# Kernel tuning notes

Hardware: AMD Instinct MI355X
Metric: run time of the kernel (lower is better)

The kernel has to match this reference:

```python
import jax, jax.numpy as jnp
import numpy as np

N = 50000      # nodes
F_IN = 2048    # raw node feature dim (pooled to 1024)
POOL = 1024
E = 1600000    # directed edges
E_SEL = 200000 # labeled edges for link prediction


def setup_inputs() -> dict:
    key = jax.random.key(0)
    ks = jax.random.split(key, 24)
    def lin(k, fin, fout):
        return jax.random.normal(k, (fin, fout), dtype=jnp.float32) / np.float32(np.sqrt(fin))
    inp = {
        "x": jax.random.normal(ks[0], (N, F_IN), dtype=jnp.float32),
        "edge_index": jax.random.randint(ks[1], (2, E), 0, N, dtype=jnp.int32),
        "mask": jax.random.randint(ks[2], (E_SEL,), 0, E, dtype=jnp.int32),
        "ln_g": jnp.ones((POOL,), jnp.float32),
        "ln_b": jnp.zeros((POOL,), jnp.float32),
        "w0": lin(ks[3], 1024, 512), "b0": jnp.zeros((512,), jnp.float32),
        "w1": lin(ks[4], 512, 128),  "b1": jnp.zeros((128,), jnp.float32),
        "w2": lin(ks[5], 128, 64),   "b2": jnp.zeros((64,), jnp.float32),
        "c1w": lin(ks[6], 64, 32),   "c1b": jnp.zeros((32,), jnp.float32),
        "c2w": lin(ks[7], 32, 16),   "c2b": jnp.zeros((16,), jnp.float32),
        "lw1": lin(ks[8], 32, 16),   "lb1": jnp.zeros((16,), jnp.float32),
        "lw2": lin(ks[9], 16, 2),    "lb2": jnp.zeros((2,), jnp.float32),
    }
    return inp


def gcn_conv(x, src, dst, W, b):
    # PyG GCNConv: add self loops, symmetric normalization D^-1/2 (A+I) D^-1/2 (x @ W) + b
    xw = x @ W
    loop = jnp.arange(N, dtype=src.dtype)
    src2 = jnp.concatenate([src, loop])
    dst2 = jnp.concatenate([dst, loop])
    deg = jax.ops.segment_sum(jnp.ones(src2.shape[0], xw.dtype), dst2, num_segments=N)
    dinv = jax.lax.rsqrt(jnp.maximum(deg, 1e-12))
    norm = dinv[src2] * dinv[dst2]              # [E+N]
    out = jax.ops.segment_sum(xw[src2] * norm[:, None], dst2, num_segments=N)
    return out + b


def reference(x, edge_index, mask, ln_g, ln_b, w0, b0, w1, b1, w2, b2,
              c1w, c1b, c2w, c2b, lw1, lb1, lw2, lb2):
    src, dst = edge_index[0], edge_index[1]
    # AdaptiveMaxPool1d(1024): exact divisor case -> max over contiguous pairs
    h = x.reshape(N, POOL, F_IN // POOL).max(axis=-1)
    # LayerNorm(1024)
    mu = h.mean(axis=-1, keepdims=True)
    var = jnp.mean(jnp.square(h - mu), axis=-1, keepdims=True)
    h = (h - mu) * jax.lax.rsqrt(var + 1e-5) * ln_g + ln_b
    h = jax.nn.elu(h @ w0 + b0)
    h = jax.nn.elu(h @ w1 + b1)
    h = jax.nn.elu(h @ w2 + b2)
    # dropout p=0.2 -> identity in eval mode
    h = jax.nn.elu(gcn_conv(h, src, dst, c1w, c1b))
    z = gcn_conv(h, src, dst, c2w, c2b)          # [N, 16]
    sel = edge_index[:, mask]                    # labeled edges
    e = jnp.concatenate([z[sel[0]], z[sel[1]]], axis=1)  # [E_SEL, 32]
    e = jax.nn.elu(e @ lw1 + lb1)
    return e @ lw2 + lb2                         # [E_SEL, 2]
```

## Files before the change

kernel.cpp:

```cpp
#include <hip/hip_runtime.h>
#include <cstdint>

using short8  = __attribute__((ext_vector_type(8))) short;
using floatx4 = __attribute__((ext_vector_type(4))) float;

__device__ __forceinline__ unsigned short f2bf(float x){
  union { float f; unsigned u; } v; v.f = x;
  unsigned r = v.u + 0x7fffu + ((v.u >> 16) & 1u);
  return (unsigned short)(r >> 16);
}

__device__ __forceinline__ float eluf(float v){ return v > 0.f ? v : expm1f(v); }

__device__ __forceinline__ void ld_g2l16(const void* g, void* l){
  __builtin_amdgcn_global_load_lds(
      (const __attribute__((address_space(1))) void*)g,
      (__attribute__((address_space(3))) void*)l, 16, 0, 0);
}

__global__ void k_tcvt(const float* __restrict__ W, unsigned short* __restrict__ Wt,
                       int K, int Ncols){
  int idx = blockIdx.x * 256 + threadIdx.x;
  if (idx >= K * Ncols) return;
  int n = idx / K, k = idx - n * K;
  Wt[idx] = f2bf(W[(size_t)k * Ncols + n]);
}

__global__ __launch_bounds__(256) void k_pool_ln(const float* __restrict__ x,
    const float* __restrict__ g, const float* __restrict__ b,
    unsigned short* __restrict__ h0){
  const int i = blockIdx.x, t = threadIdx.x;
  const float4* xr = (const float4*)(x + (size_t)i * 2048);
  float4 va = xr[2 * t], vb = xr[2 * t + 1];
  float v0 = fmaxf(va.x, va.y), v1 = fmaxf(va.z, va.w);
  float v2 = fmaxf(vb.x, vb.y), v3 = fmaxf(vb.z, vb.w);
  float s  = v0 + v1 + v2 + v3;
  float s2 = v0*v0 + v1*v1 + v2*v2 + v3*v3;
  #pragma unroll
  for (int off = 32; off > 0; off >>= 1){
    s  += __shfl_down(s, off);
    s2 += __shfl_down(s2, off);
  }
  __shared__ float ps[4], ps2[4];
  int w = t >> 6;
  if ((t & 63) == 0){ ps[w] = s; ps2[w] = s2; }
  __syncthreads();
  float S  = ps[0] + ps[1] + ps[2] + ps[3];
  float S2 = ps2[0] + ps2[1] + ps2[2] + ps2[3];
  float mu   = S * (1.f / 1024.f);
  float var  = S2 * (1.f / 1024.f) - mu * mu;
  float rstd = rsqrtf(var + 1e-5f);
  float4 g4 = ((const float4*)g)[t];
  float4 b4 = ((const float4*)b)[t];
  ushort4 o;
  o.x = f2bf((v0 - mu) * rstd * g4.x + b4.x);
  o.y = f2bf((v1 - mu) * rstd * g4.y + b4.y);
  o.z = f2bf((v2 - mu) * rstd * g4.z + b4.z);
  o.w = f2bf((v3 - mu) * rstd * g4.w + b4.w);
  *(ushort4*)(h0 + (size_t)i * 1024 + t * 4) = o;
}

__global__ __launch_bounds__(256) void k_gemm(const unsigned short* __restrict__ A,
    const unsigned short* __restrict__ Bt, const float* __restrict__ bias,
    unsigned short* __restrict__ C, int M, int K, int N){
  __shared__ __align__(16) unsigned short lA[128 * 64];
  __shared__ __align__(16) unsigned short lB[128 * 64];
  const int tid  = threadIdx.x;
  const int lane = tid & 63;
  const int w    = tid >> 6;
  const int wm = w >> 1, wn = w & 1;
  const int m0 = blockIdx.x * 128;
  const int n0 = blockIdx.y * 128;
  const int q = lane >> 4, ml = lane & 15;
  floatx4 acc[4][4] = {};
  const int nKB = K >> 6;
  for (int kb = 0; kb < nKB; ++kb){
    #pragma unroll
    for (int i = 0; i < 4; ++i){
      int cpos = (w * 4 + i) * 64 + lane;
      int row  = cpos >> 3;
      int p    = cpos & 7;
      int cc   = p ^ (row & 7);
      int ar   = m0 + row; ar = ar < M ? ar : M - 1;
      ld_g2l16(A  + (size_t)ar        * K + (kb * 64 + cc * 8), &lA[(w * 4 + i) * 512]);
      ld_g2l16(Bt + (size_t)(n0 + row) * K + (kb * 64 + cc * 8), &lB[(w * 4 + i) * 512]);
    }
    __syncthreads();
    #pragma unroll
    for (int kk = 0; kk < 2; ++kk){
      short8 af[4], bfr[4];
      #pragma unroll
      for (int mi = 0; mi < 4; ++mi){
        int row = wm * 64 + mi * 16 + ml;
        int p   = (kk * 4 + q) ^ (row & 7);
        af[mi] = *(const short8*)&lA[row * 64 + p * 8];
      }
      #pragma unroll
      for (int ni = 0; ni < 4; ++ni){
        int row = wn * 64 + ni * 16 + ml;
        int p   = (kk * 4 + q) ^ (row & 7);
        bfr[ni] = *(const short8*)&lB[row * 64 + p * 8];
      }
      #pragma unroll
      for (int mi = 0; mi < 4; ++mi)
        #pragma unroll
        for (int ni = 0; ni < 4; ++ni)
          acc[mi][ni] = __builtin_amdgcn_mfma_f32_16x16x32_bf16(af[mi], bfr[ni], acc[mi][ni], 0, 0, 0);
    }
    __syncthreads();
  }
  #pragma unroll
  for (int mi = 0; mi < 4; ++mi){
    #pragma unroll
    for (int ni = 0; ni < 4; ++ni){
      int gc = n0 + wn * 64 + ni * 16 + ml;
      float bv = bias[gc];
      #pragma unroll
      for (int r = 0; r < 4; ++r){
        int gr = m0 + wm * 64 + mi * 16 + q * 4 + r;
        if (gr < M){
          float v = acc[mi][ni][r] + bv;
          v = v > 0.f ? v : expm1f(v);
          C[(size_t)gr * N + gc] = f2bf(v);
        }
      }
    }
  }
}

__global__ __launch_bounds__(256) void k_h3(const unsigned short* __restrict__ h2,
    const unsigned short* __restrict__ w2t, const float* __restrict__ b2,
    unsigned short* __restrict__ h3, int M){
  int gw = (blockIdx.x * 256 + threadIdx.x) >> 6;
  int lane = threadIdx.x & 63;
  int r0 = gw * 16;
  if (r0 >= M) return;
  int ml = lane & 15, q = lane >> 4;
  int ar = r0 + ml; if (ar >= M) ar = M - 1;
  floatx4 acc[4] = {};
  #pragma unroll
  for (int kk = 0; kk < 4; ++kk){
    short8 a = *(const short8*)&h2[(size_t)ar * 128 + kk * 32 + q * 8];
    #pragma unroll
    for (int ni = 0; ni < 4; ++ni){
      short8 bb = *(const short8*)&w2t[(ni * 16 + ml) * 128 + kk * 32 + q * 8];
      acc[ni] = __builtin_amdgcn_mfma_f32_16x16x32_bf16(a, bb, acc[ni], 0, 0, 0);
    }
  }
  #pragma unroll
  for (int ni = 0; ni < 4; ++ni){
    int gc = ni * 16 + ml;
    float bv = b2[gc];
    #pragma unroll
    for (int r = 0; r < 4; ++r){
      int gr = r0 + q * 4 + r;
      if (gr < M) h3[(size_t)gr * 64 + gc] = f2bf(eluf(acc[ni][r] + bv));
    }
  }
}

__global__ __launch_bounds__(256) void k_xs1(const unsigned short* __restrict__ h3,
    const unsigned short* __restrict__ c1wt, const float* __restrict__ dinv,
    float* __restrict__ xs1, int M){
  int gw = (blockIdx.x * 256 + threadIdx.x) >> 6;
  int lane = threadIdx.x & 63;
  int r0 = gw * 16;
  if (r0 >= M) return;
  int ml = lane & 15, q = lane >> 4;
  int ar = r0 + ml; if (ar >= M) ar = M - 1;
  floatx4 acc[2] = {};
  #pragma unroll
  for (int kk = 0; kk < 2; ++kk){
    short8 a = *(const short8*)&h3[(size_t)ar * 64 + kk * 32 + q * 8];
    #pragma unroll
    for (int ni = 0; ni < 2; ++ni){
      short8 bb = *(const short8*)&c1wt[(ni * 16 + ml) * 64 + kk * 32 + q * 8];
      acc[ni] = __builtin_amdgcn_mfma_f32_16x16x32_bf16(a, bb, acc[ni], 0, 0, 0);
    }
  }
  #pragma unroll
  for (int ni = 0; ni < 2; ++ni){
    int gc = ni * 16 + ml;
    #pragma unroll
    for (int r = 0; r < 4; ++r){
      int gr = r0 + q * 4 + r;
      if (gr < M) xs1[(size_t)gr * 32 + gc] = acc[ni][r] * dinv[gr];
    }
  }
}

__global__ __launch_bounds__(256) void k_fin1(const float* __restrict__ acc1,
    const float* __restrict__ c1b, const unsigned short* __restrict__ c2wt,
    const float* __restrict__ dinv, float* __restrict__ xs2, int M){
  int gw = (blockIdx.x * 256 + threadIdx.x) >> 6;
  int lane = threadIdx.x & 63;
  int r0 = gw * 16;
  if (r0 >= M) return;
  int ml = lane & 15, q = lane >> 4;
  int ar = r0 + ml; if (ar >= M) ar = M - 1;
  float dr = dinv[ar];
  short8 a;
  #pragma unroll
  for (int j = 0; j < 8; ++j){
    float v = dr * acc1[(size_t)ar * 32 + q * 8 + j] + c1b[q * 8 + j];
    a[j] = (short)f2bf(eluf(v));
  }
  short8 bb = *(const short8*)&c2wt[ml * 32 + q * 8];
  floatx4 c = {0.f, 0.f, 0.f, 0.f};
  c = __builtin_amdgcn_mfma_f32_16x16x32_bf16(a, bb, c, 0, 0, 0);
  #pragma unroll
  for (int r = 0; r < 4; ++r){
    int gr = r0 + q * 4 + r;
    if (gr < M) xs2[(size_t)gr * 16 + ml] = c[r] * dinv[gr];
  }
}

__global__ void k_zero2(int* __restrict__ a, int* __restrict__ b, int Nn){
  int i = blockIdx.x * 256 + threadIdx.x;
  if (i < Nn){ a[i] = 0; b[i] = 0; }
}
__global__ void k_degi(const int* __restrict__ ei, int* __restrict__ deg, int E){
  int e = blockIdx.x * 256 + threadIdx.x;
  if (e < E) atomicAdd(&deg[ei[E + e]], 1);
}
__global__ void k_dinv(const int* __restrict__ deg, float* __restrict__ dinv, int Nn){
  int i = blockIdx.x * 256 + threadIdx.x;
  if (i < Nn) dinv[i] = rsqrtf((float)deg[i] + 1.0f);
}
__global__ __launch_bounds__(256) void k_scan1(const int* __restrict__ deg,
    int* __restrict__ ptr, int* __restrict__ btot, int Nn){
  __shared__ int s[256];
  int b = blockIdx.x, t = threadIdx.x, i = b * 256 + t;
  int v = (i < Nn) ? deg[i] : 0;
  s[t] = v; __syncthreads();
  #pragma unroll
  for (int off = 1; off < 256; off <<= 1){
    int x = (t >= off) ? s[t - off] : 0;
    __syncthreads();
    s[t] += x; __syncthreads();
  }
  if (i < Nn) ptr[i] = s[t] - v;
  if (t == 255) btot[b] = s[255];
}
__global__ __launch_bounds__(256) void k_scan2(int* __restrict__ btot, int nb){
  __shared__ int s[256];
  int t = threadIdx.x;
  int v = (t < nb) ? btot[t] : 0;
  s[t] = v; __syncthreads();
  #pragma unroll
  for (int off = 1; off < 256; off <<= 1){
    int x = (t >= off) ? s[t - off] : 0;
    __syncthreads();
    s[t] += x; __syncthreads();
  }
  if (t < nb) btot[t] = s[t] - v;
}
__global__ void k_scan3(int* __restrict__ ptr, const int* __restrict__ btot, int Nn){
  int i = blockIdx.x * 256 + threadIdx.x;
  if (i < Nn) ptr[i] += btot[blockIdx.x >> 0 ? i >> 8 : 0];
}
__global__ void k_fill(const int* __restrict__ ei, const int* __restrict__ ptr,
                       int* __restrict__ cnt, int* __restrict__ csr, int E){
  int e = blockIdx.x * 256 + threadIdx.x;
  if (e >= E) return;
  int d = ei[E + e];
  int pos = ptr[d] + atomicAdd(&cnt[d], 1);
  csr[pos] = ei[e];
}

template <int C4, int LOG2C4>
__global__ __launch_bounds__(256) void k_gather(const int* __restrict__ csr,
    const int* __restrict__ ptr, const int* __restrict__ deg,
    const float* __restrict__ xs, float* __restrict__ acc, int M){
  int wid = (blockIdx.x * 256 + threadIdx.x) >> 6;
  if (wid >= M) return;
  int lane = threadIdx.x & 63;
  int g = lane >> LOG2C4;
  int c = lane & (C4 - 1);
  const int EPI = 64 >> LOG2C4;
  int start = ptr[wid], n = deg[wid];
  float4 a = {0.f, 0.f, 0.f, 0.f};
  for (int j = g; j < n; j += EPI){
    int s = csr[start + j];
    float4 v = *(const float4*)&xs[(size_t)s * (C4 * 4) + c * 4];
    a.x += v.x; a.y += v.y; a.z += v.z; a.w += v.w;
  }
  #pragma unroll
  for (int off = C4; off < 64; off <<= 1){
    a.x += __shfl_xor(a.x, off);
    a.y += __shfl_xor(a.y, off);
    a.z += __shfl_xor(a.z, off);
    a.w += __shfl_xor(a.w, off);
  }
  if (g == 0){
    float4 self = *(const float4*)&xs[(size_t)wid * (C4 * 4) + c * 4];
    float4 o = {a.x + self.x, a.y + self.y, a.z + self.z, a.w + self.w};
    *(float4*)&acc[(size_t)wid * (C4 * 4) + c * 4] = o;
  }
}

__global__ void k_fin2(const float* __restrict__ acc2, const float* __restrict__ c2b,
                       const float* __restrict__ dinv, float* __restrict__ z, int M){
  int gid = blockIdx.x * 256 + threadIdx.x;
  if (gid >= M * 16) return;
  int i = gid >> 4, c = gid & 15;
  z[gid] = dinv[i] * acc2[gid] + c2b[c];
}

__global__ __launch_bounds__(256) void k_edge(const int* __restrict__ ei,
    const int* __restrict__ mask, const float* __restrict__ z,
    const float* __restrict__ lw1, const float* __restrict__ lb1,
    const float* __restrict__ lw2, const float* __restrict__ lb2,
    float* __restrict__ out, int nsel, int E){
  __shared__ float w1s[512], b1s[16], w2s[32], b2s[2];
  int t = threadIdx.x;
  for (int idx = t; idx < 512; idx += 256) w1s[idx] = lw1[idx];
  if (t < 16) b1s[t] = lb1[t];
  if (t < 32) w2s[t] = lw2[t];
  if (t < 2)  b2s[t] = lb2[t];
  __syncthreads();
  int j = blockIdx.x * 256 + t;
  if (j >= nsel) return;
  int m = mask[j];
  int s = ei[m], d = ei[E + m];
  float e[32];
  const float4* zs = (const float4*)(z + (size_t)s * 16);
  const float4* zd = (const float4*)(z + (size_t)d * 16);
  #pragma unroll
  for (int k4 = 0; k4 < 4; ++k4){
    float4 v = zs[k4];
    e[k4 * 4 + 0] = v.x; e[k4 * 4 + 1] = v.y; e[k4 * 4 + 2] = v.z; e[k4 * 4 + 3] = v.w;
  }
  #pragma unroll
  for (int k4 = 0; k4 < 4; ++k4){
    float4 v = zd[k4];
    e[16 + k4 * 4 + 0] = v.x; e[16 + k4 * 4 + 1] = v.y;
    e[16 + k4 * 4 + 2] = v.z; e[16 + k4 * 4 + 3] = v.w;
  }
  float o[16];
  #pragma unroll
  for (int oo = 0; oo < 16; ++oo){
    float acc = b1s[oo];
    #pragma unroll
    for (int ii = 0; ii < 32; ++ii) acc += e[ii] * w1s[ii * 16 + oo];
    o[oo] = eluf(acc);
  }
  float r0 = b2s[0], r1 = b2s[1];
  #pragma unroll
  for (int oo = 0; oo < 16; ++oo){ r0 += o[oo] * w2s[oo * 2]; r1 += o[oo] * w2s[oo * 2 + 1]; }
  out[(size_t)j * 2]     = r0;
  out[(size_t)j * 2 + 1] = r1;
}

extern "C" void kernel_launch(void* const* d_in, const int* in_sizes, int n_in,
                              void* d_out, int out_size, void* d_ws, size_t ws_size,
                              hipStream_t stream){
  const float* x    = (const float*)d_in[0];
  const int*   ei   = (const int*)d_in[1];
  const int*   mask = (const int*)d_in[2];
  const float* ln_g = (const float*)d_in[3];
  const float* ln_b = (const float*)d_in[4];
  const float* w0   = (const float*)d_in[5];
  const float* b0   = (const float*)d_in[6];
  const float* w1   = (const float*)d_in[7];
  const float* b1   = (const float*)d_in[8];
  const float* w2   = (const float*)d_in[9];
  const float* b2   = (const float*)d_in[10];
  const float* c1w  = (const float*)d_in[11];
  const float* c1b  = (const float*)d_in[12];
  const float* c2w  = (const float*)d_in[13];
  const float* c2b  = (const float*)d_in[14];
  const float* lw1  = (const float*)d_in[15];
  const float* lb1  = (const float*)d_in[16];
  const float* lw2  = (const float*)d_in[17];
  const float* lb2  = (const float*)d_in[18];
  float* out = (float*)d_out;

  const int N    = in_sizes[0] / 2048;
  const int E    = in_sizes[1] / 2;
  const int NSEL = in_sizes[2];
  const int NB   = (N + 255) / 256;

  char* ws = (char*)d_ws;
  size_t o = 0;
  unsigned short* h2   = (unsigned short*)(ws + o); o += (size_t)N * 256;
  float* xs1  = (float*)(ws + o); o += (size_t)N * 128;
  float* acc1 = (float*)(ws + o); o += (size_t)N * 128;
  float* xs2  = (float*)(ws + o); o += (size_t)N * 64;
  float* acc2 = (float*)(ws + o); o += (size_t)N * 64;
  float* z    = (float*)(ws + o); o += (size_t)N * 64;
  int*   degi = (int*)(ws + o);   o += (size_t)N * 4;
  float* dinv = (float*)(ws + o); o += (size_t)N * 4;
  int*   ptr  = (int*)(ws + o);   o += (size_t)N * 4;
  int*   cnt  = (int*)(ws + o);   o += (size_t)N * 4;
  int*   btot = (int*)(ws + o);   o += 256 * 4;
  int*   csr  = (int*)(ws + o);   o += (size_t)E * 4;
  unsigned short* h3 = (unsigned short*)(ws + o);   o += (size_t)N * 128;
  unsigned short* h0 = (unsigned short*)(ws + 0);
  size_t base2 = (size_t)N * 2048;
  unsigned short* h1   = (unsigned short*)(ws + base2);        o = base2 + (size_t)N * 1024;
  unsigned short* w0t  = (unsigned short*)(ws + o);            o += 1024 * 512 * 2;
  unsigned short* w1t  = (unsigned short*)(ws + o);            o += 512 * 128 * 2;
  unsigned short* w2t  = (unsigned short*)(ws + o);            o += 128 * 64 * 2;
  unsigned short* c1wt = (unsigned short*)(ws + o);            o += 64 * 32 * 2;
  unsigned short* c2wt = (unsigned short*)(ws + o);

  k_tcvt<<<(1024 * 512 + 255) / 256, 256, 0, stream>>>(w0, w0t, 1024, 512);
  k_tcvt<<<(512 * 128 + 255) / 256, 256, 0, stream>>>(w1, w1t, 512, 128);
  k_tcvt<<<(128 * 64 + 255) / 256, 256, 0, stream>>>(w2, w2t, 128, 64);
  k_tcvt<<<(64 * 32 + 255) / 256, 256, 0, stream>>>(c1w, c1wt, 64, 32);
  k_tcvt<<<(32 * 16 + 255) / 256, 256, 0, stream>>>(c2w, c2wt, 32, 16);

  k_pool_ln<<<N, 256, 0, stream>>>(x, ln_g, ln_b, h0);

  k_gemm<<<dim3((N + 127) / 128, 4), 256, 0, stream>>>(h0, w0t, b0, h1, N, 1024, 512);

  k_zero2<<<NB, 256, 0, stream>>>(degi, cnt, N);
  k_degi<<<(E + 255) / 256, 256, 0, stream>>>(ei, degi, E);
  k_dinv<<<NB, 256, 0, stream>>>(degi, dinv, N);
  k_scan1<<<NB, 256, 0, stream>>>(degi, ptr, btot, N);
  k_scan2<<<1, 256, 0, stream>>>(btot, NB);
  k_scan3<<<NB, 256, 0, stream>>>(ptr, btot, N);
  k_fill<<<(E + 255) / 256, 256, 0, stream>>>(ei, ptr, cnt, csr, E);

  k_gemm<<<dim3((N + 127) / 128, 1), 256, 0, stream>>>(h1, w1t, b1, h2, N, 512, 128);

  int nwaves = (N + 15) / 16;
  int wblocks = (nwaves + 3) / 4;
  k_h3<<<wblocks, 256, 0, stream>>>(h2, w2t, b2, h3, N);

  k_xs1<<<wblocks, 256, 0, stream>>>(h3, c1wt, dinv, xs1, N);
  k_gather<8, 3><<<(N + 3) / 4, 256, 0, stream>>>(csr, ptr, degi, xs1, acc1, N);
  k_fin1<<<wblocks, 256, 0, stream>>>(acc1, c1b, c2wt, dinv, xs2, N);

  k_gather<4, 2><<<(N + 3) / 4, 256, 0, stream>>>(csr, ptr, degi, xs2, acc2, N);
  k_fin2<<<(N * 16 + 255) / 256, 256, 0, stream>>>(acc2, c2b, dinv, z, N);

  k_edge<<<(NSEL + 255) / 256, 256, 0, stream>>>(ei, mask, z, lw1, lb1, lw2, lb2,
                                                 out, NSEL, E);
}
```

Baseline: 974.1 us.

## Fuse small MLP layers and GCN epilogues into fewer kernels

Merges the 512->128, 128->64 and 64->32 layers into one kernel that keeps intermediate activations in shared memory, so the h2 and h3 round-trips through global memory disappear. The first gather now applies the bias, ELU and c2 projection in fp32, and the second gather applies the output epilogue directly. The weight conversions and zeroing are packed into one prep launch, and dinv is computed inside the scan kernel. Together these cut launch count and intermediate traffic, at the cost of more shared-memory use and register pressure in the fused kernel.

```diff
diff --git a/kernel.cpp b/kernel.cpp
--- a/kernel.cpp
+++ b/kernel.cpp
@@ -18,12 +18,31 @@
       (__attribute__((address_space(3))) void*)l, 16, 0, 0);
 }
 
-__global__ void k_tcvt(const float* __restrict__ W, unsigned short* __restrict__ Wt,
-                       int K, int Ncols){
+__device__ __forceinline__ void tcv(const float* W, unsigned short* Wt, int K, int Nc, int i){
+  int n = i / K, k = i - n * K;
+  Wt[i] = f2bf(W[(size_t)k * Nc + n]);
+}
+__global__ void k_prep(const float* __restrict__ w0, const float* __restrict__ w1,
+                       const float* __restrict__ w2, const float* __restrict__ c1w,
+                       const float* __restrict__ c2w,
+                       unsigned short* __restrict__ w0t, unsigned short* __restrict__ w1t,
+                       unsigned short* __restrict__ w2t, unsigned short* __restrict__ c1wt,
+                       unsigned short* __restrict__ c2wt,
+                       int* __restrict__ degi, int* __restrict__ cnt, int N){
   int idx = blockIdx.x * 256 + threadIdx.x;
-  if (idx >= K * Ncols) return;
-  int n = idx / K, k = idx - n * K;
-  Wt[idx] = f2bf(W[(size_t)k * Ncols + n]);
+  if (idx < 524288){ tcv(w0, w0t, 1024, 512, idx); return; }
+  idx -= 524288;
+  if (idx < 65536){ tcv(w1, w1t, 512, 128, idx); return; }
+  idx -= 65536;
+  if (idx < 8192){ tcv(w2, w2t, 128, 64, idx); return; }
+  idx -= 8192;
+  if (idx < 2048){ tcv(c1w, c1wt, 64, 32, idx); return; }
+  idx -= 2048;
+  if (idx < 512){ tcv(c2w, c2wt, 32, 16, idx); return; }
+  idx -= 512;
+  if (idx < N){ degi[idx] = 0; return; }
+  idx -= N;
+  if (idx < N){ cnt[idx] = 0; }
 }
 
 __global__ __launch_bounds__(256) void k_pool_ln(const float* __restrict__ x,
@@ -128,110 +147,143 @@
   }
 }
 
-__global__ __launch_bounds__(256) void k_h3(const unsigned short* __restrict__ h2,
+#define H2S 136
+#define H3S 72
+__global__ __launch_bounds__(256) void k_mlp2(const unsigned short* __restrict__ h1,
+    const unsigned short* __restrict__ w1t, const float* __restrict__ b1,
     const unsigned short* __restrict__ w2t, const float* __restrict__ b2,
-    unsigned short* __restrict__ h3, int M){
-  int gw = (blockIdx.x * 256 + threadIdx.x) >> 6;
-  int lane = threadIdx.x & 63;
-  int r0 = gw * 16;
-  if (r0 >= M) return;
-  int ml = lane & 15, q = lane >> 4;
-  int ar = r0 + ml; if (ar >= M) ar = M - 1;
-  floatx4 acc[4] = {};
-  #pragma unroll
-  for (int kk = 0; kk < 4; ++kk){
-    short8 a = *(const short8*)&h2[(size_t)ar * 128 + kk * 32 + q * 8];
-    #pragma unroll
-    for (int ni = 0; ni < 4; ++ni){
-      short8 bb = *(const short8*)&w2t[(ni * 16 + ml) * 128 + kk * 32 + q * 8];
-      acc[ni] = __builtin_amdgcn_mfma_f32_16x16x32_bf16(a, bb, acc[ni], 0, 0, 0);
-    }
-  }
-  #pragma unroll
-  for (int ni = 0; ni < 4; ++ni){
-    int gc = ni * 16 + ml;
-    float bv = b2[gc];
-    #pragma unroll
-    for (int r = 0; r < 4; ++r){
-      int gr = r0 + q * 4 + r;
-      if (gr < M) h3[(size_t)gr * 64 + gc] = f2bf(eluf(acc[ni][r] + bv));
-    }
-  }
-}
-
-__global__ __launch_bounds__(256) void k_xs1(const unsigned short* __restrict__ h3,
     const unsigned short* __restrict__ c1wt, const float* __restrict__ dinv,
     float* __restrict__ xs1, int M){
-  int gw = (blockIdx.x * 256 + threadIdx.x) >> 6;
-  int lane = threadIdx.x & 63;
-  int r0 = gw * 16;
-  if (r0 >= M) return;
-  int ml = lane & 15, q = lane >> 4;
-  int ar = r0 + ml; if (ar >= M) ar = M - 1;
-  floatx4 acc[2] = {};
+  __shared__ __align__(16) unsigned short sm[128 * H2S + 128 * H3S];
+  unsigned short* lA  = sm;
+  unsigned short* lB  = sm + 8192;
+  unsigned short* h2s = sm;
+  unsigned short* h3s = sm + 128 * H2S;
+  const int tid  = threadIdx.x;
+  const int lane = tid & 63;
+  const int w    = tid >> 6;
+  const int wm = w >> 1, wn = w & 1;
+  const int m0 = blockIdx.x * 128;
+  const int q = lane >> 4, ml = lane & 15;
+  floatx4 acc[4][4] = {};
+  for (int kb = 0; kb < 8; ++kb){
+    #pragma unroll
+    for (int i = 0; i < 4; ++i){
+      int cpos = (w * 4 + i) * 64 + lane;
+      int row  = cpos >> 3;
+      int p    = cpos & 7;
+      int cc   = p ^ (row & 7);
+      int ar   = m0 + row; ar = ar < M ? ar : M - 1;
+      ld_g2l16(h1  + (size_t)ar  * 512 + (kb * 64 + cc * 8), &lA[(w * 4 + i) * 512]);
+      ld_g2l16(w1t + (size_t)row * 512 + (kb * 64 + cc * 8), &lB[(w * 4 + i) * 512]);
+    }
+    __syncthreads();
+    #pragma unroll
+    for (int kk = 0; kk < 2; ++kk){
+      short8 af[4], bfr[4];
+      #pragma unroll
+      for (int mi = 0; mi < 4; ++mi){
+        int row = wm * 64 + mi * 16 + ml;
+        int p   = (kk * 4 + q) ^ (row & 7);
+        af[mi] = *(const short8*)&lA[row * 64 + p * 8];
+      }
+      #pragma unroll
+      for (int ni = 0; ni < 4; ++ni){
+        int row = wn * 64 + ni * 16 + ml;
+        int p   = (kk * 4 + q) ^ (row & 7);
+        bfr[ni] = *(const short8*)&lB[row * 64 + p * 8];
+      }
+      #pragma unroll
+      for (int mi = 0; mi < 4; ++mi)
+        #pragma unroll
+        for (int ni = 0; ni < 4; ++ni)
+          acc[mi][ni] = __builtin_amdgcn_mfma_f32_16x16x32_bf16(af[mi], bfr[ni], acc[mi][ni], 0, 0, 0);
+    }
+    __syncthreads();
+  }
+  #pragma unroll
+  for (int mi = 0; mi < 4; ++mi){
+    #pragma unroll
+    for (int ni = 0; ni < 4; ++ni){
+      int col = wn * 64 + ni * 16 + ml;
+      float bv = b1[col];
+      #pragma unroll
+      for (int r = 0; r < 4; ++r){
+        int row = wm * 64 + mi * 16 + q * 4 + r;
+        h2s[row * H2S + col] = f2bf(eluf(acc[mi][ni][r] + bv));
+      }
+    }
+  }
+  __syncthreads();
+  const int r0 = w * 32;
+  floatx4 acc3[2][4] = {};
+  #pragma unroll
+  for (int kk = 0; kk < 4; ++kk){
+    short8 a3[2];
+    #pragma unroll
+    for (int mi = 0; mi < 2; ++mi)
+      a3[mi] = *(const short8*)&h2s[(r0 + mi * 16 + ml) * H2S + kk * 32 + q * 8];
+    #pragma unroll
+    for (int ni = 0; ni < 4; ++ni){
+      short8 b3 = *(const short8*)&w2t[(ni * 16 + ml) * 128 + kk * 32 + q * 8];
+      #pragma unroll
+      for (int mi = 0; mi < 2; ++mi)
+        acc3[mi][ni] = __builtin_amdgcn_mfma_f32_16x16x32_bf16(a3[mi], b3, acc3[mi][ni], 0, 0, 0);
+    }
+  }
+  #pragma unroll
+  for (int mi = 0; mi < 2; ++mi){
+    #pragma unroll
+    for (int ni = 0; ni < 4; ++ni){
+      int col = ni * 16 + ml;
+      float bv = b2[col];
+      #pragma unroll
+      for (int r = 0; r < 4; ++r){
+        int row = r0 + mi * 16 + q * 4 + r;
+        h3s[row * H3S + col] = f2bf(eluf(acc3[mi][ni][r] + bv));
+      }
+    }
+  }
+  __syncthreads();
+  floatx4 accx[2][2] = {};
   #pragma unroll
   for (int kk = 0; kk < 2; ++kk){
-    short8 a = *(const short8*)&h3[(size_t)ar * 64 + kk * 32 + q * 8];
+    short8 ax[2];
+    #pragma unroll
+    for (int mi = 0; mi < 2; ++mi)
+      ax[mi] = *(const short8*)&h3s[(r0 + mi * 16 + ml) * H3S + kk * 32 + q * 8];
     #pragma unroll
     for (int ni = 0; ni < 2; ++ni){
-      short8 bb = *(const short8*)&c1wt[(ni * 16 + ml) * 64 + kk * 32 + q * 8];
-      acc[ni] = __builtin_amdgcn_mfma_f32_16x16x32_bf16(a, bb, acc[ni], 0, 0, 0);
-    }
-  }
-  #pragma unroll
-  for (int ni = 0; ni < 2; ++ni){
-    int gc = ni * 16 + ml;
-    #pragma unroll
-    for (int r = 0; r < 4; ++r){
-      int gr = r0 + q * 4 + r;
-      if (gr < M) xs1[(size_t)gr * 32 + gc] = acc[ni][r] * dinv[gr];
-    }
-  }
-}
-
-__global__ __launch_bounds__(256) void k_fin1(const float* __restrict__ acc1,
-    const float* __restrict__ c1b, const unsigned short* __restrict__ c2wt,
-    const float* __restrict__ dinv, float* __restrict__ xs2, int M){
-  int gw = (blockIdx.x * 256 + threadIdx.x) >> 6;
-  int lane = threadIdx.x & 63;
-  int r0 = gw * 16;
-  if (r0 >= M) return;
-  int ml = lane & 15, q = lane >> 4;
-  int ar = r0 + ml; if (ar >= M) ar = M - 1;
-  float dr = dinv[ar];
-  short8 a;
-  #pragma unroll
-  for (int j = 0; j < 8; ++j){
-    float v = dr * acc1[(size_t)ar * 32 + q * 8 + j] + c1b[q * 8 + j];
-    a[j] = (short)f2bf(eluf(v));
-  }
-  short8 bb = *(const short8*)&c2wt[ml * 32 + q * 8];
-  floatx4 c = {0.f, 0.f, 0.f, 0.f};
-  c = __builtin_amdgcn_mfma_f32_16x16x32_bf16(a, bb, c, 0, 0, 0);
-  #pragma unroll
-  for (int r = 0; r < 4; ++r){
-    int gr = r0 + q * 4 + r;
-    if (gr < M) xs2[(size_t)gr * 16 + ml] = c[r] * dinv[gr];
-  }
-}
-
-__global__ void k_zero2(int* __restrict__ a, int* __restrict__ b, int Nn){
-  int i = blockIdx.x * 256 + threadIdx.x;
-  if (i < Nn){ a[i] = 0; b[i] = 0; }
-}
+      short8 bx = *(const short8*)&c1wt[(ni * 16 + ml) * 64 + kk * 32 + q * 8];
+      #pragma unroll
+      for (int mi = 0; mi < 2; ++mi)
+        accx[mi][ni] = __builtin_amdgcn_mfma_f32_16x16x32_bf16(ax[mi], bx, accx[mi][ni], 0, 0, 0);
+    }
+  }
+  #pragma unroll
+  for (int mi = 0; mi < 2; ++mi){
+    #pragma unroll
+    for (int ni = 0; ni < 2; ++ni){
+      int col = ni * 16 + ml;
+      #pragma unroll
+      for (int r = 0; r < 4; ++r){
+        int gr = m0 + r0 + mi * 16 + q * 4 + r;
+        if (gr < M) xs1[(size_t)gr * 32 + col] = accx[mi][ni][r] * dinv[gr];
+      }
+    }
+  }
+}
+
 __global__ void k_degi(const int* __restrict__ ei, int* __restrict__ deg, int E){
   int e = blockIdx.x * 256 + threadIdx.x;
   if (e < E) atomicAdd(&deg[ei[E + e]], 1);
 }
-__global__ void k_dinv(const int* __restrict__ deg, float* __restrict__ dinv, int Nn){
-  int i = blockIdx.x * 256 + threadIdx.x;
-  if (i < Nn) dinv[i] = rsqrtf((float)deg[i] + 1.0f);
-}
 __global__ __launch_bounds__(256) void k_scan1(const int* __restrict__ deg,
-    int* __restrict__ ptr, int* __restrict__ btot, int Nn){
+    int* __restrict__ ptr, int* __restrict__ btot, float* __restrict__ dinv, int Nn){
   __shared__ int s[256];
   int b = blockIdx.x, t = threadIdx.x, i = b * 256 + t;
   int v = (i < Nn) ? deg[i] : 0;
+  if (i < Nn) dinv[i] = rsqrtf((float)v + 1.0f);
   s[t] = v; __syncthreads();
   #pragma unroll
   for (int off = 1; off < 256; off <<= 1){
@@ -257,7 +309,7 @@
 }
 __global__ void k_scan3(int* __restrict__ ptr, const int* __restrict__ btot, int Nn){
   int i = blockIdx.x * 256 + threadIdx.x;
-  if (i < Nn) ptr[i] += btot[blockIdx.x >> 0 ? i >> 8 : 0];
+  if (i < Nn) ptr[i] += btot[i >> 8];
 }
 __global__ void k_fill(const int* __restrict__ ei, const int* __restrict__ ptr,
                        int* __restrict__ cnt, int* __restrict__ csr, int E){
@@ -268,43 +320,96 @@
   csr[pos] = ei[e];
 }
 
-template <int C4, int LOG2C4>
-__global__ __launch_bounds__(256) void k_gather(const int* __restrict__ csr,
+__global__ __launch_bounds__(256) void k_gather1(const int* __restrict__ csr,
     const int* __restrict__ ptr, const int* __restrict__ deg,
-    const float* __restrict__ xs, float* __restrict__ acc, int M){
+    const float* __restrict__ xs1, const float* __restrict__ c1b,
+    const float* __restrict__ c2w, const float* __restrict__ dinv,
+    float* __restrict__ xs2, int M){
   int wid = (blockIdx.x * 256 + threadIdx.x) >> 6;
   if (wid >= M) return;
   int lane = threadIdx.x & 63;
-  int g = lane >> LOG2C4;
-  int c = lane & (C4 - 1);
-  const int EPI = 64 >> LOG2C4;
+  int g = lane >> 3, c = lane & 7;
   int start = ptr[wid], n = deg[wid];
   float4 a = {0.f, 0.f, 0.f, 0.f};
-  for (int j = g; j < n; j += EPI){
+  for (int j = g; j < n; j += 8){
     int s = csr[start + j];
-    float4 v = *(const float4*)&xs[(size_t)s * (C4 * 4) + c * 4];
+    float4 v = *(const float4*)&xs1[(size_t)s * 32 + c * 4];
     a.x += v.x; a.y += v.y; a.z += v.z; a.w += v.w;
   }
   #pragma unroll
-  for (int off = C4; off < 64; off <<= 1){
+  for (int off = 8; off < 64; off <<= 1){
     a.x += __shfl_xor(a.x, off);
     a.y += __shfl_xor(a.y, off);
     a.z += __shfl_xor(a.z, off);
     a.w += __shfl_xor(a.w, off);
   }
+  float4 self = *(const float4*)&xs1[(size_t)wid * 32 + c * 4];
+  a.x += self.x; a.y += self.y; a.z += self.z; a.w += self.w;
+  float dv = dinv[wid];
+  float h4[4];
+  h4[0] = eluf(dv * a.x + c1b[c * 4 + 0]);
+  h4[1] = eluf(dv * a.y + c1b[c * 4 + 1]);
+  h4[2] = eluf(dv * a.z + c1b[c * 4 + 2]);
+  h4[3] = eluf(dv * a.w + c1b[c * 4 + 3]);
+  float p[16];
+  #pragma unroll
+  for (int j = 0; j < 16; ++j) p[j] = 0.f;
+  #pragma unroll
+  for (int u = 0; u < 4; ++u){
+    const float4* wr = (const float4*)&c2w[(c * 4 + u) * 16];
+    #pragma unroll
+    for (int j4 = 0; j4 < 4; ++j4){
+      float4 wv = wr[j4];
+      p[j4 * 4 + 0] += h4[u] * wv.x;
+      p[j4 * 4 + 1] += h4[u] * wv.y;
+      p[j4 * 4 + 2] += h4[u] * wv.z;
+      p[j4 * 4 + 3] += h4[u] * wv.w;
+    }
+  }
+  #pragma unroll
+  for (int off = 1; off < 8; off <<= 1)
+    #pragma unroll
+    for (int j = 0; j < 16; ++j) p[j] += __shfl_xor(p[j], off);
+  if (lane == 0){
+    float4* po = (float4*)&xs2[(size_t)wid * 16];
+    #pragma unroll
+    for (int j4 = 0; j4 < 4; ++j4){
+      float4 v = {dv * p[j4*4+0], dv * p[j4*4+1], dv * p[j4*4+2], dv * p[j4*4+3]};
+      po[j4] = v;
+    }
+  }
+}
+
+__global__ __launch_bounds__(256) void k_gather2(const int* __restrict__ csr,
+    const int* __restrict__ ptr, const int* __restrict__ deg,
+    const float* __restrict__ xs2, const float* __restrict__ c2b,
+    const float* __restrict__ dinv, float* __restrict__ z, int M){
+  int wid = (blockIdx.x * 256 + threadIdx.x) >> 6;
+  if (wid >= M) return;
+  int lane = threadIdx.x & 63;
+  int g = lane >> 2, c = lane & 3;
+  int start = ptr[wid], n = deg[wid];
+  float4 a = {0.f, 0.f, 0.f, 0.f};
+  for (int j = g; j < n; j += 16){
+    int s = csr[start + j];
+    float4 v = *(const float4*)&xs2[(size_t)s * 16 + c * 4];
+    a.x += v.x; a.y += v.y; a.z += v.z; a.w += v.w;
+  }
+  #pragma unroll
+  for (int off = 4; off < 64; off <<= 1){
+    a.x += __shfl_xor(a.x, off);
+    a.y += __shfl_xor(a.y, off);
+    a.z += __shfl_xor(a.z, off);
+    a.w += __shfl_xor(a.w, off);
+  }
   if (g == 0){
-    float4 self = *(const float4*)&xs[(size_t)wid * (C4 * 4) + c * 4];
-    float4 o = {a.x + self.x, a.y + self.y, a.z + self.z, a.w + self.w};
-    *(float4*)&acc[(size_t)wid * (C4 * 4) + c * 4] = o;
-  }
-}
-
-__global__ void k_fin2(const float* __restrict__ acc2, const float* __restrict__ c2b,
-                       const float* __restrict__ dinv, float* __restrict__ z, int M){
-  int gid = blockIdx.x * 256 + threadIdx.x;
-  if (gid >= M * 16) return;
-  int i = gid >> 4, c = gid & 15;
-  z[gid] = dinv[i] * acc2[gid] + c2b[c];
+    float4 self = *(const float4*)&xs2[(size_t)wid * 16 + c * 4];
+    float dv = dinv[wid];
+    const float4 cb = ((const float4*)c2b)[c];
+    float4 o = {dv * (a.x + self.x) + cb.x, dv * (a.y + self.y) + cb.y,
+                dv * (a.z + self.z) + cb.z, dv * (a.w + self.w) + cb.w};
+    *(float4*)&z[(size_t)wid * 16 + c * 4] = o;
+  }
 }
 
 __global__ __launch_bounds__(256) void k_edge(const int* __restrict__ ei,
@@ -383,59 +488,36 @@
 
   char* ws = (char*)d_ws;
   size_t o = 0;
-  unsigned short* h2   = (unsigned short*)(ws + o); o += (size_t)N * 256;
-  float* xs1  = (float*)(ws + o); o += (size_t)N * 128;
-  float* acc1 = (float*)(ws + o); o += (size_t)N * 128;
-  float* xs2  = (float*)(ws + o); o += (size_t)N * 64;
-  float* acc2 = (float*)(ws + o); o += (size_t)N * 64;
-  float* z    = (float*)(ws + o); o += (size_t)N * 64;
+  unsigned short* h0   = (unsigned short*)(ws + o); o += (size_t)N * 1024 * 2;
+  unsigned short* h1   = (unsigned short*)(ws + o); o += (size_t)N * 512 * 2;
+  unsigned short* w0t  = (unsigned short*)(ws + o); o += 1024 * 512 * 2;
+  unsigned short* w1t  = (unsigned short*)(ws + o); o += 512 * 128 * 2;
+  unsigned short* w2t  = (unsigned short*)(ws + o); o += 128 * 64 * 2;
+  unsigned short* c1wt = (unsigned short*)(ws + o); o += 64 * 32 * 2;
+  unsigned short* c2wt = (unsigned short*)(ws + o); o += 32 * 16 * 2;
   int*   degi = (int*)(ws + o);   o += (size_t)N * 4;
+  int*   cnt  = (int*)(ws + o);   o += (size_t)N * 4;
+  int*   ptr  = (int*)(ws + o);   o += (size_t)N * 4;
   float* dinv = (float*)(ws + o); o += (size_t)N * 4;
-  int*   ptr  = (int*)(ws + o);   o += (size_t)N * 4;
-  int*   cnt  = (int*)(ws + o);   o += (size_t)N * 4;
   int*   btot = (int*)(ws + o);   o += 256 * 4;
   int*   csr  = (int*)(ws + o);   o += (size_t)E * 4;
-  unsigned short* h3 = (unsigned short*)(ws + o);   o += (size_t)N * 128;
-  unsigned short* h0 = (unsigned short*)(ws + 0);
-  size_t base2 = (size_t)N * 2048;
-  unsigned short* h1   = (unsigned short*)(ws + base2);        o = base2 + (size_t)N * 1024;
-  unsigned short* w0t  = (unsigned short*)(ws + o);            o += 1024 * 512 * 2;
-  unsigned short* w1t  = (unsigned short*)(ws + o);            o += 512 * 128 * 2;
-  unsigned short* w2t  = (unsigned short*)(ws + o);            o += 128 * 64 * 2;
-  unsigned short* c1wt = (unsigned short*)(ws + o);            o += 64 * 32 * 2;
-  unsigned short* c2wt = (unsigned short*)(ws + o);
-
-  k_tcvt<<<(1024 * 512 + 255) / 256, 256, 0, stream>>>(w0, w0t, 1024, 512);
-  k_tcvt<<<(512 * 128 + 255) / 256, 256, 0, stream>>>(w1, w1t, 512, 128);
-  k_tcvt<<<(128 * 64 + 255) / 256, 256, 0, stream>>>(w2, w2t, 128, 64);
-  k_tcvt<<<(64 * 32 + 255) / 256, 256, 0, stream>>>(c1w, c1wt, 64, 32);
-  k_tcvt<<<(32 * 16 + 255) / 256, 256, 0, stream>>>(c2w, c2wt, 32, 16);
-
+  float* xs1  = (float*)(ws + o); o += (size_t)N * 32 * 4;
+  float* xs2  = (float*)(ws + o); o += (size_t)N * 16 * 4;
+  float* z    = (float*)(ws + o); o += (size_t)N * 16 * 4;
+
+  int prep_n = 524288 + 65536 + 8192 + 2048 + 512 + 2 * N;
+  k_prep<<<(prep_n + 255) / 256, 256, 0, stream>>>(w0, w1, w2, c1w, c2w,
+      w0t, w1t, w2t, c1wt, c2wt, degi, cnt, N);
   k_pool_ln<<<N, 256, 0, stream>>>(x, ln_g, ln_b, h0);
-
   k_gemm<<<dim3((N + 127) / 128, 4), 256, 0, stream>>>(h0, w0t, b0, h1, N, 1024, 512);
-
-  k_zero2<<<NB, 256, 0, stream>>>(degi, cnt, N);
   k_degi<<<(E + 255) / 256, 256, 0, stream>>>(ei, degi, E);
-  k_dinv<<<NB, 256, 0, stream>>>(degi, dinv, N);
-  k_scan1<<<NB, 256, 0, stream>>>(degi, ptr, btot, N);
+  k_scan1<<<NB, 256, 0, stream>>>(degi, ptr, btot, dinv, N);
   k_scan2<<<1, 256, 0, stream>>>(btot, NB);
   k_scan3<<<NB, 256, 0, stream>>>(ptr, btot, N);
   k_fill<<<(E + 255) / 256, 256, 0, stream>>>(ei, ptr, cnt, csr, E);
-
-  k_gemm<<<dim3((N + 127) / 128, 1), 256, 0, stream>>>(h1, w1t, b1, h2, N, 512, 128);
-
-  int nwaves = (N + 15) / 16;
-  int wblocks = (nwaves + 3) / 4;
-  k_h3<<<wblocks, 256, 0, stream>>>(h2, w2t, b2, h3, N);
-
-  k_xs1<<<wblocks, 256, 0, stream>>>(h3, c1wt, dinv, xs1, N);
-  k_gather<8, 3><<<(N + 3) / 4, 256, 0, stream>>>(csr, ptr, degi, xs1, acc1, N);
-  k_fin1<<<wblocks, 256, 0, stream>>>(acc1, c1b, c2wt, dinv, xs2, N);
-
-  k_gather<4, 2><<<(N + 3) / 4, 256, 0, stream>>>(csr, ptr, degi, xs2, acc2, N);
-  k_fin2<<<(N * 16 + 255) / 256, 256, 0, stream>>>(acc2, c2b, dinv, z, N);
-
+  k_mlp2<<<(N + 127) / 128, 256, 0, stream>>>(h1, w1t, b1, w2t, b2, c1wt, dinv, xs1, N);
+  k_gather1<<<(N + 3) / 4, 256, 0, stream>>>(csr, ptr, degi, xs1, c1b, c2w, dinv, xs2, N);
+  k_gather2<<<(N + 3) / 4, 256, 0, stream>>>(csr, ptr, degi, xs2, c2b, dinv, z, N);
   k_edge<<<(NSEL + 255) / 256, 256, 0, stream>>>(ei, mask, z, lw1, lb1, lw2, lb2,
                                                  out, NSEL, E);
 }
```

Result: slower. 1.033 ms (+6.1%).
